# Performance work log

Hardware: AMD Instinct MI355X
Metric: run time of the kernel (lower is better)

## Reference

```python
import jax, jax.numpy as jnp
import numpy as np

K = 16          # neighbors per node
EPS = 1e-5      # BatchNorm eps
BN_SCALE = 1.0 / np.sqrt(1.0 + EPS)  # eval BN with running mean=0, var=1


def _knn_idx(x, k):
    # x: [B, N, d] -> idx [B, N, k] of k nearest neighbors (self excluded)
    sq = jnp.sum(x * x, axis=-1)                               # [B, N]
    d2 = sq[:, :, None] + sq[:, None, :] - 2.0 * jnp.einsum('bnd,bmd->bnm', x, x)
    n = x.shape[1]
    d2 = jnp.where(jnp.eye(n, dtype=bool)[None], jnp.inf, d2)  # no self loops
    _, idx = jax.lax.top_k(-d2, k)
    return idx


def _edge_conv(x, idx, W, b, g, be):
    # PyG EdgeConv: max_j MLP([x_i, x_j - x_i]); MLP = Linear+BN(eval)+ReLU
    xj = jax.vmap(lambda xb, ib: xb[ib])(x, idx)               # [B, N, k, d]
    xi = x[:, :, None, :]
    m = jnp.concatenate([jnp.broadcast_to(xi, xj.shape), xj - xi], axis=-1)
    h = m @ W + b                                              # [B, N, k, out]
    h = g * (h * BN_SCALE) + be                                # eval BatchNorm
    h = jax.nn.relu(h)
    return jnp.max(h, axis=2)                                  # scatter-max over k


def setup_inputs() -> dict:
    key = jax.random.key(0)
    ks = jax.random.split(key, 16)
    B, N, D, C = 128, 256, 6, 12

    def w(k_, shape, fan_in):
        return (jax.random.normal(k_, shape, jnp.float32) / np.sqrt(fan_in)).astype(jnp.float32)

    inp = {
        'x':   jax.random.normal(ks[0], (B, N, D), jnp.float32),
        'W1':  w(ks[1], (2 * 6, 64), 12),   'b1': jnp.zeros((64,), jnp.float32),
        'g1':  jnp.ones((64,), jnp.float32), 'be1': jnp.zeros((64,), jnp.float32),
        'W2':  w(ks[2], (2 * 64, 128), 128), 'b2': jnp.zeros((128,), jnp.float32),
        'g2':  jnp.ones((128,), jnp.float32), 'be2': jnp.zeros((128,), jnp.float32),
        'W3':  w(ks[3], (2 * 128, 256), 256), 'b3': jnp.zeros((256,), jnp.float32),
        'g3':  jnp.ones((256,), jnp.float32), 'be3': jnp.zeros((256,), jnp.float32),
        'Wf1': w(ks[4], (256, 128), 256),    'bf1': jnp.zeros((128,), jnp.float32),
        'gf':  jnp.ones((128,), jnp.float32), 'bef': jnp.zeros((128,), jnp.float32),
        'Wf2': w(ks[5], (128, C), 128),      'bf2': jnp.zeros((C,), jnp.float32),
    }
    return inp


def reference(x, W1, b1, g1, be1, W2, b2, g2, be2, W3, b3, g3, be3,
              Wf1, bf1, gf, bef, Wf2, bf2):
    h = _edge_conv(x, _knn_idx(x, K), W1, b1, g1, be1)   # [B, N, 64]
    h = _edge_conv(h, _knn_idx(h, K), W2, b2, g2, be2)   # [B, N, 128]
    h = _edge_conv(h, _knn_idx(h, K), W3, b3, g3, be3)   # [B, N, 256]
    p = jnp.max(h, axis=1)                               # global_max_pool [B, 256]
    f = jax.nn.relu(gf * ((p @ Wf1 + bf1) * BN_SCALE) + bef)
    return f @ Wf2 + bf2                                 # [B, num_classes]
```

## Files before the change

kernel.cpp:

```cpp
#include <hip/hip_runtime.h>
#include <cstdint>
#include <cstddef>

#define KNN 16
#define NPTS 256
#define NBATCH 128

static constexpr float BN_SCALE_F = 0.9999950000374997f;

__device__ inline unsigned int f32_ord(float f) {
    unsigned int u = __float_as_uint(f);
    return (u & 0x80000000u) ? ~u : (u | 0x80000000u);
}

__device__ __forceinline__ int wmap(int n) { return n + 4 * (n >> 4); }

template<int D>
__global__ __launch_bounds__(256) void sq_kernel(const float* __restrict__ x,
                                                 float* __restrict__ sq) {
    const int t = blockIdx.x * 256 + threadIdx.x;
    const float* r = x + (size_t)t * D;
    float s = 0.f;
    #pragma unroll
    for (int d = 0; d < D; ++d) s = fmaf(r[d], r[d], s);
    sq[t] = s;
}

template<int D>
__global__ __launch_bounds__(256) void gram_kernel(const float* __restrict__ x,
                                                   const float* __restrict__ sq,
                                                   float* __restrict__ d2) {
    constexpr int KS = (D >= 16) ? 16 : D;
    const int t  = threadIdx.x;
    const int tx = t & 15, ty = t >> 4;
    const int b    = blockIdx.x >> 4;
    const int tile = blockIdx.x & 15;
    const int i0 = (tile & 3) * 64;
    const int j0 = (tile >> 2) * 64;
    const int base = b * NPTS;

    __shared__ float As[KS][68];
    __shared__ float Bs[KS][68];

    float acc[4][4] = {};
    for (int k0 = 0; k0 < D; k0 += KS) {
        if constexpr (D % 16 == 0) {
            const int r  = t >> 2;
            const int cq = (t & 3) * 4;
            const float4 va = *(const float4*)(x + (size_t)(base + i0 + r) * D + k0 + cq);
            const float4 vb = *(const float4*)(x + (size_t)(base + j0 + r) * D + k0 + cq);
            As[cq + 0][r] = va.x; As[cq + 1][r] = va.y;
            As[cq + 2][r] = va.z; As[cq + 3][r] = va.w;
            Bs[cq + 0][r] = vb.x; Bs[cq + 1][r] = vb.y;
            Bs[cq + 2][r] = vb.z; Bs[cq + 3][r] = vb.w;
        } else {
            for (int e = t; e < 64 * KS; e += 256) {
                const int r = e / KS, c = e % KS;
                As[c][r] = x[(size_t)(base + i0 + r) * D + k0 + c];
                Bs[c][r] = x[(size_t)(base + j0 + r) * D + k0 + c];
            }
        }
        __syncthreads();
        #pragma unroll
        for (int kk = 0; kk < KS; ++kk) {
            const float4 av = *(const float4*)&As[kk][ty * 4];
            const float4 bv = *(const float4*)&Bs[kk][tx * 4];
            const float am[4] = {av.x, av.y, av.z, av.w};
            const float bm[4] = {bv.x, bv.y, bv.z, bv.w};
            #pragma unroll
            for (int m = 0; m < 4; ++m)
                #pragma unroll
                for (int n = 0; n < 4; ++n)
                    acc[m][n] = fmaf(am[m], bm[n], acc[m][n]);
        }
        __syncthreads();
    }

    float sqi[4], sqj[4];
    #pragma unroll
    for (int m = 0; m < 4; ++m) {
        sqi[m] = sq[base + i0 + ty * 4 + m];
        sqj[m] = sq[base + j0 + tx * 4 + m];
    }
    #pragma unroll
    for (int m = 0; m < 4; ++m) {
        const int gi = i0 + ty * 4 + m;
        float v[4];
        #pragma unroll
        for (int n = 0; n < 4; ++n) {
            v[n] = (sqi[m] + sqj[n]) - 2.f * acc[m][n];
            if (gi == j0 + tx * 4 + n) v[n] = INFINITY;
        }
        float4* dst = (float4*)(d2 + ((size_t)b << 16) + (size_t)gi * NPTS + j0 + tx * 4);
        *dst = make_float4(v[0], v[1], v[2], v[3]);
    }
}

__global__ __launch_bounds__(256) void topk_kernel(const float* __restrict__ d2,
                                                   int* __restrict__ idx) {
    const int t = threadIdx.x;
    const int p = t >> 3;
    const int q = t & 7;
    const int ig = blockIdx.x * 32 + p;
    const float* row = d2 + (size_t)ig * NPTS;

    unsigned long long L[16];
    #pragma unroll
    for (int r = 0; r < 16; ++r) L[r] = ~0ull;

    const int jb = q * 32;
    #pragma unroll
    for (int jj = 0; jj < 32; jj += 4) {
        const float4 v4 = *(const float4*)(row + jb + jj);
        const float vv[4] = {v4.x, v4.y, v4.z, v4.w};
        #pragma unroll
        for (int e = 0; e < 4; ++e) {
            const unsigned long long key =
                ((unsigned long long)f32_ord(vv[e]) << 32) |
                (unsigned int)(jb + jj + e);
            #pragma unroll
            for (int r = 15; r >= 1; --r)
                L[r] = (key < L[r]) ? ((key < L[r - 1]) ? L[r - 1] : key) : L[r];
            L[0] = (key < L[0]) ? key : L[0];
        }
    }

    __shared__ unsigned long long K[256][17];
    #pragma unroll
    for (int r = 0; r < 16; ++r) K[t][r] = L[r];
    __syncthreads();

    if (t < 32) {
        const int pp  = t;
        const int igo = blockIdx.x * 32 + pp;
        int h[8];
        unsigned long long v[8];
        #pragma unroll
        for (int c = 0; c < 8; ++c) { h[c] = 0; v[c] = K[pp * 8 + c][0]; }
        int outj[16];
        #pragma unroll
        for (int r = 0; r < 16; ++r) {
            unsigned long long best = v[0];
            #pragma unroll
            for (int c = 1; c < 8; ++c) best = (v[c] < best) ? v[c] : best;
            outj[r] = (int)(unsigned int)(best & 0xffffffffull);
            #pragma unroll
            for (int c = 0; c < 8; ++c) {
                const bool hit = (v[c] == best);
                const int hn = h[c] + (hit ? 1 : 0);
                const unsigned long long nv = K[pp * 8 + c][hn & 15];
                v[c] = hit ? ((hn < 16) ? nv : ~0ull) : v[c];
                h[c] = hn;
            }
        }
        int4* op = (int4*)(idx + (size_t)igo * KNN);
        op[0] = make_int4(outj[0],  outj[1],  outj[2],  outj[3]);
        op[1] = make_int4(outj[4],  outj[5],  outj[6],  outj[7]);
        op[2] = make_int4(outj[8],  outj[9],  outj[10], outj[11]);
        op[3] = make_int4(outj[12], outj[13], outj[14], outj[15]);
    }
}

template<int D, int C>
__global__ __launch_bounds__(256) void mlp_gemm_kernel(
        const float* __restrict__ x, const float* __restrict__ W,
        const float* __restrict__ bias, const float* __restrict__ g,
        const float* __restrict__ be,
        float* __restrict__ A, float* __restrict__ Bv) {
    constexpr int BM = 128;
    constexpr int KT = (D >= 16) ? 16 : D;
    const int t  = threadIdx.x;
    const int m0 = blockIdx.x * BM;
    const int n0 = blockIdx.y * 128;
    const int tx = t & 15;
    const int ty = t >> 4;

    __shared__ float Xs[KT][BM + 4];
    __shared__ float Ws[KT][160];

    float acc[8][8] = {};

    for (int k0 = 0; k0 < D; k0 += KT) {
        if constexpr (D % 16 == 0) {
            const int r  = t >> 1;
            const int cq = (t & 1) * 8;
            const float* src = x + (size_t)(m0 + r) * D + k0 + cq;
            const float4 v0 = *(const float4*)(src);
            const float4 v1 = *(const float4*)(src + 4);
            Xs[cq + 0][r] = v0.x; Xs[cq + 1][r] = v0.y;
            Xs[cq + 2][r] = v0.z; Xs[cq + 3][r] = v0.w;
            Xs[cq + 4][r] = v1.x; Xs[cq + 5][r] = v1.y;
            Xs[cq + 6][r] = v1.z; Xs[cq + 7][r] = v1.w;
        } else {
            for (int e = t; e < BM * KT; e += 256) {
                const int r = e / KT, c = e % KT;
                Xs[c][r] = x[(size_t)(m0 + r) * D + k0 + c];
            }
        }
        if constexpr (D % 16 == 0) {
            const int wk = t >> 4;
            const int nq = (t & 15) * 8;
            const int mb = wmap(nq);
            const int gn = n0 + nq;
            const int kr = k0 + wk;
            if (gn < C) {
                const float* pt = W + (size_t)kr * C + gn;
                const float* pb = W + (size_t)(D + kr) * C + gn;
                const float4 t0 = *(const float4*)(pt);
                const float4 t1 = *(const float4*)(pt + 4);
                const float4 b0 = *(const float4*)(pb);
                const float4 b1 = *(const float4*)(pb + 4);
                *(float4*)&Ws[wk][mb]     = make_float4(t0.x - b0.x, t0.y - b0.y,
                                                        t0.z - b0.z, t0.w - b0.w);
                *(float4*)&Ws[wk][mb + 4] = make_float4(t1.x - b1.x, t1.y - b1.y,
                                                        t1.z - b1.z, t1.w - b1.w);
            } else {
                const float* pb = W + (size_t)(D + kr) * C + (gn - C);
                *(float4*)&Ws[wk][mb]     = *(const float4*)(pb);
                *(float4*)&Ws[wk][mb + 4] = *(const float4*)(pb + 4);
            }
        } else {
            for (int e = t; e < KT * 128; e += 256) {
                const int k = e >> 7, n = e & 127;
                const int gn = n0 + n, kr = k0 + k;
                Ws[k][wmap(n)] = (gn < C)
                    ? W[(size_t)kr * C + gn] - W[(size_t)(D + kr) * C + gn]
                    : W[(size_t)(D + kr) * C + (gn - C)];
            }
        }
        __syncthreads();

        const int mc = wmap(tx * 8);
        #pragma unroll
        for (int kk = 0; kk < KT; ++kk) {
            float xm[8], wn[8];
            *(float4*)&xm[0] = *(const float4*)&Xs[kk][ty * 8];
            *(float4*)&xm[4] = *(const float4*)&Xs[kk][ty * 8 + 4];
            *(float4*)&wn[0] = *(const float4*)&Ws[kk][mc];
            *(float4*)&wn[4] = *(const float4*)&Ws[kk][mc + 4];
            #pragma unroll
            for (int m = 0; m < 8; ++m)
                #pragma unroll
                for (int n = 0; n < 8; ++n)
                    acc[m][n] = fmaf(xm[m], wn[n], acc[m][n]);
        }
        __syncthreads();
    }

    const int gn = n0 + tx * 8;
    if (gn < C) {
        float fac[8];
        #pragma unroll
        for (int e = 0; e < 8; ++e) fac[e] = g[gn + e] * BN_SCALE_F;
        #pragma unroll
        for (int m = 0; m < 8; ++m) {
            float o[8];
            #pragma unroll
            for (int e = 0; e < 8; ++e) o[e] = fac[e] * acc[m][e];
            float* dst = A + (size_t)(m0 + ty * 8 + m) * C + gn;
            *(float4*)(dst)     = make_float4(o[0], o[1], o[2], o[3]);
            *(float4*)(dst + 4) = make_float4(o[4], o[5], o[6], o[7]);
        }
    } else {
        const int cb = gn - C;
        float fac[8], bb[8], bee[8];
        #pragma unroll
        for (int e = 0; e < 8; ++e) {
            fac[e] = g[cb + e] * BN_SCALE_F;
            bb[e]  = bias[cb + e];
            bee[e] = be[cb + e];
        }
        #pragma unroll
        for (int m = 0; m < 8; ++m) {
            float o[8];
            #pragma unroll
            for (int e = 0; e < 8; ++e)
                o[e] = fmaf(fac[e], acc[m][e] + bb[e], bee[e]);
            float* dst = Bv + (size_t)(m0 + ty * 8 + m) * C + cb;
            *(float4*)(dst)     = make_float4(o[0], o[1], o[2], o[3]);
            *(float4*)(dst + 4) = make_float4(o[4], o[5], o[6], o[7]);
        }
    }
}

template<int C>
__global__ __launch_bounds__(C) void combine_kernel(
        const float* A, const float* __restrict__ Bv,
        const int* __restrict__ idx, float* out) {
    const int bi = blockIdx.x;
    const int c  = threadIdx.x;
    __shared__ int nbr[KNN];
    if (c < KNN) nbr[c] = idx[(size_t)bi * KNN + c];
    __syncthreads();
    const int b0 = bi & ~255;
    float mx = -INFINITY;
    #pragma unroll
    for (int kk = 0; kk < KNN; ++kk)
        mx = fmaxf(mx, Bv[(size_t)(b0 + nbr[kk]) * C + c]);
    float a = A[(size_t)bi * C + c];
    out[(size_t)bi * C + c] = fmaxf(a + mx, 0.f);
}

__global__ __launch_bounds__(256) void head_kernel(
        const float* __restrict__ h3, const float* __restrict__ Wf1,
        const float* __restrict__ bf1, const float* __restrict__ gf,
        const float* __restrict__ bef, const float* __restrict__ Wf2,
        const float* __restrict__ bf2, float* __restrict__ out) {
    const int b   = blockIdx.x;
    const int tid = threadIdx.x;
    __shared__ float p[256];
    __shared__ float f[128];
    const float* hb = h3 + (size_t)b * NPTS * 256;
    float mx = -INFINITY;
    for (int n = 0; n < NPTS; ++n) mx = fmaxf(mx, hb[(size_t)n * 256 + tid]);
    p[tid] = mx;
    __syncthreads();
    if (tid < 128) {
        float acc = bf1[tid];
        for (int d = 0; d < 256; ++d)
            acc = fmaf(p[d], Wf1[(size_t)d * 128 + tid], acc);
        float v = gf[tid] * (acc * BN_SCALE_F) + bef[tid];
        f[tid] = fmaxf(v, 0.f);
    }
    __syncthreads();
    if (tid < 12) {
        float acc = bf2[tid];
        for (int d = 0; d < 128; ++d)
            acc = fmaf(f[d], Wf2[(size_t)d * 12 + tid], acc);
        out[(size_t)b * 12 + tid] = acc;
    }
}

extern "C" void kernel_launch(void* const* d_in, const int* in_sizes, int n_in,
                              void* d_out, int out_size, void* d_ws, size_t ws_size,
                              hipStream_t stream) {
    const float* x   = (const float*)d_in[0];
    const float* W1  = (const float*)d_in[1];
    const float* b1  = (const float*)d_in[2];
    const float* g1  = (const float*)d_in[3];
    const float* be1 = (const float*)d_in[4];
    const float* W2  = (const float*)d_in[5];
    const float* b2  = (const float*)d_in[6];
    const float* g2  = (const float*)d_in[7];
    const float* be2 = (const float*)d_in[8];
    const float* W3  = (const float*)d_in[9];
    const float* b3  = (const float*)d_in[10];
    const float* g3  = (const float*)d_in[11];
    const float* be3 = (const float*)d_in[12];
    const float* Wf1 = (const float*)d_in[13];
    const float* bf1 = (const float*)d_in[14];
    const float* gf  = (const float*)d_in[15];
    const float* bef = (const float*)d_in[16];
    const float* Wf2 = (const float*)d_in[17];
    const float* bf2 = (const float*)d_in[18];
    float* out = (float*)d_out;

    char* ws = (char*)d_ws;
    const size_t idx_bytes = (size_t)NBATCH * NPTS * KNN * sizeof(int);
    const size_t reg_bytes = (size_t)NBATCH * NPTS * 256 * sizeof(float);
    int*   idx = (int*)ws;
    float* R1  = (float*)(ws + idx_bytes);
    float* R2  = (float*)(ws + idx_bytes + reg_bytes);
    float* R3  = (float*)(ws + idx_bytes + 2 * reg_bytes);
    float* sqb = (float*)(ws + idx_bytes + 3 * reg_bytes);

    const int BN = NBATCH * NPTS;
    const int GRAM_GRID = NBATCH * 16;
    const int TOPK_GRID = BN / 32;
    const int MB = BN / 128;

    sq_kernel<6><<<BN / 256, 256, 0, stream>>>(x, sqb);
    gram_kernel<6><<<GRAM_GRID, 256, 0, stream>>>(x, sqb, R3);
    topk_kernel<<<TOPK_GRID, 256, 0, stream>>>(R3, idx);
    mlp_gemm_kernel<6, 64><<<dim3(MB, 1), 256, 0, stream>>>(
        x, W1, b1, g1, be1, R1, R2);
    combine_kernel<64><<<BN, 64, 0, stream>>>(R1, R2, idx, R1);

    sq_kernel<64><<<BN / 256, 256, 0, stream>>>(R1, sqb);
    gram_kernel<64><<<GRAM_GRID, 256, 0, stream>>>(R1, sqb, R3);
    topk_kernel<<<TOPK_GRID, 256, 0, stream>>>(R3, idx);
    mlp_gemm_kernel<64, 128><<<dim3(MB, 2), 256, 0, stream>>>(
        R1, W2, b2, g2, be2, R2, R3);
    combine_kernel<128><<<BN, 128, 0, stream>>>(R2, R3, idx, R2);

    sq_kernel<128><<<BN / 256, 256, 0, stream>>>(R2, sqb);
    gram_kernel<128><<<GRAM_GRID, 256, 0, stream>>>(R2, sqb, R1);
    topk_kernel<<<TOPK_GRID, 256, 0, stream>>>(R1, idx);
    mlp_gemm_kernel<128, 256><<<dim3(MB, 4), 256, 0, stream>>>(
        R2, W3, b3, g3, be3, R3, R1);
    combine_kernel<256><<<BN, 256, 0, stream>>>(R3, R1, idx, R3);

    head_kernel<<<NBATCH, 256, 0, stream>>>(R3, Wf1, bf1, gf, bef, Wf2, bf2, out);
}
```

Baseline: 482.1 us.

## Fuse distance matrix and top-k selection into one kNN kernel

Replaces the separate gram kernel (which wrote the full 256x256 distance matrix per batch to global memory) and the top-k kernel (which read it back) with a single kernel. Each block owns 64 query rows, loops over four 64-column tiles, stages distances in shared memory, and keeps per-thread sorted top-16 lists using 32-bit keys plus separate indices, then merges four partial lists per row. This removes the d2 global round trip and a launch per layer. In exchange the grid shrinks from 2048 to 512 blocks, shared memory use grows, and register pressure rises, which may reduce occupancy.

Measured after the change: 463.3 us. -3.9%, faster.

```diff
diff --git a/kernel.cpp b/kernel.cpp
--- a/kernel.cpp
+++ b/kernel.cpp
@@ -27,133 +27,143 @@
 }
 
 template<int D>
-__global__ __launch_bounds__(256) void gram_kernel(const float* __restrict__ x,
-                                                   const float* __restrict__ sq,
-                                                   float* __restrict__ d2) {
+__global__ __launch_bounds__(256) void knn_fused_kernel(
+        const float* __restrict__ x, const float* __restrict__ sq,
+        int* __restrict__ idx) {
     constexpr int KS = (D >= 16) ? 16 : D;
     const int t  = threadIdx.x;
     const int tx = t & 15, ty = t >> 4;
-    const int b    = blockIdx.x >> 4;
-    const int tile = blockIdx.x & 15;
-    const int i0 = (tile & 3) * 64;
-    const int j0 = (tile >> 2) * 64;
+    const int sr = t >> 2, sc = t & 3;
+    const int b  = blockIdx.x >> 2;
+    const int i0 = (blockIdx.x & 3) * 64;
     const int base = b * NPTS;
 
     __shared__ float As[KS][68];
     __shared__ float Bs[KS][68];
-
-    float acc[4][4] = {};
-    for (int k0 = 0; k0 < D; k0 += KS) {
-        if constexpr (D % 16 == 0) {
-            const int r  = t >> 2;
-            const int cq = (t & 3) * 4;
-            const float4 va = *(const float4*)(x + (size_t)(base + i0 + r) * D + k0 + cq);
-            const float4 vb = *(const float4*)(x + (size_t)(base + j0 + r) * D + k0 + cq);
-            As[cq + 0][r] = va.x; As[cq + 1][r] = va.y;
-            As[cq + 2][r] = va.z; As[cq + 3][r] = va.w;
-            Bs[cq + 0][r] = vb.x; Bs[cq + 1][r] = vb.y;
-            Bs[cq + 2][r] = vb.z; Bs[cq + 3][r] = vb.w;
-        } else {
-            for (int e = t; e < 64 * KS; e += 256) {
-                const int r = e / KS, c = e % KS;
-                As[c][r] = x[(size_t)(base + i0 + r) * D + k0 + c];
-                Bs[c][r] = x[(size_t)(base + j0 + r) * D + k0 + c];
+    __shared__ float d2L[64][65];
+    __shared__ unsigned short Mi[64][68];
+
+    unsigned int Lv[16], Li[16];
+    #pragma unroll
+    for (int q = 0; q < 16; ++q) { Lv[q] = 0xFFFFFFFFu; Li[q] = 0u; }
+
+    for (int jt = 0; jt < 4; ++jt) {
+        const int j0 = jt * 64;
+        float acc[4][4] = {};
+        for (int k0 = 0; k0 < D; k0 += KS) {
+            if constexpr (D % 16 == 0) {
+                const int r  = t >> 2;
+                const int cq = (t & 3) * 4;
+                const float4 va = *(const float4*)(x + (size_t)(base + i0 + r) * D + k0 + cq);
+                const float4 vb = *(const float4*)(x + (size_t)(base + j0 + r) * D + k0 + cq);
+                As[cq + 0][r] = va.x; As[cq + 1][r] = va.y;
+                As[cq + 2][r] = va.z; As[cq + 3][r] = va.w;
+                Bs[cq + 0][r] = vb.x; Bs[cq + 1][r] = vb.y;
+                Bs[cq + 2][r] = vb.z; Bs[cq + 3][r] = vb.w;
+            } else {
+                for (int e = t; e < 64 * KS; e += 256) {
+                    const int r = e / KS, c = e % KS;
+                    As[c][r] = x[(size_t)(base + i0 + r) * D + k0 + c];
+                    Bs[c][r] = x[(size_t)(base + j0 + r) * D + k0 + c];
+                }
+            }
+            __syncthreads();
+            #pragma unroll
+            for (int kk = 0; kk < KS; ++kk) {
+                const float4 av = *(const float4*)&As[kk][ty * 4];
+                const float4 bv = *(const float4*)&Bs[kk][tx * 4];
+                const float am[4] = {av.x, av.y, av.z, av.w};
+                const float bm[4] = {bv.x, bv.y, bv.z, bv.w};
+                #pragma unroll
+                for (int m = 0; m < 4; ++m)
+                    #pragma unroll
+                    for (int n = 0; n < 4; ++n)
+                        acc[m][n] = fmaf(am[m], bm[n], acc[m][n]);
+            }
+            __syncthreads();
+        }
+
+        float sqi[4], sqj[4];
+        #pragma unroll
+        for (int m = 0; m < 4; ++m) {
+            sqi[m] = sq[base + i0 + ty * 4 + m];
+            sqj[m] = sq[base + j0 + tx * 4 + m];
+        }
+        #pragma unroll
+        for (int m = 0; m < 4; ++m) {
+            const int gi = i0 + ty * 4 + m;
+            #pragma unroll
+            for (int n = 0; n < 4; ++n) {
+                float v = (sqi[m] + sqj[n]) - 2.f * acc[m][n];
+                if (gi == j0 + tx * 4 + n) v = INFINITY;
+                d2L[ty * 4 + m][tx * 4 + n] = v;
             }
         }
         __syncthreads();
-        #pragma unroll
-        for (int kk = 0; kk < KS; ++kk) {
-            const float4 av = *(const float4*)&As[kk][ty * 4];
-            const float4 bv = *(const float4*)&Bs[kk][tx * 4];
-            const float am[4] = {av.x, av.y, av.z, av.w};
-            const float bm[4] = {bv.x, bv.y, bv.z, bv.w};
-            #pragma unroll
-            for (int m = 0; m < 4; ++m)
-                #pragma unroll
-                for (int n = 0; n < 4; ++n)
-                    acc[m][n] = fmaf(am[m], bm[n], acc[m][n]);
-        }
-        __syncthreads();
-    }
-
-    float sqi[4], sqj[4];
+
+        #pragma unroll
+        for (int i = 0; i < 16; ++i) {
+            const unsigned int v = f32_ord(d2L[sr][sc * 16 + i]);
+            const unsigned int j = (unsigned int)(j0 + sc * 16 + i);
+            #pragma unroll
+            for (int q = 15; q >= 1; --q) {
+                const bool a = v < Lv[q];
+                const bool c = v < Lv[q - 1];
+                Lv[q] = a ? (c ? Lv[q - 1] : v) : Lv[q];
+                Li[q] = a ? (c ? Li[q - 1] : j) : Li[q];
+            }
+            const bool a0 = v < Lv[0];
+            Lv[0] = a0 ? v : Lv[0];
+            Li[0] = a0 ? j : Li[0];
+        }
+    }
+
+    __syncthreads();
     #pragma unroll
-    for (int m = 0; m < 4; ++m) {
-        sqi[m] = sq[base + i0 + ty * 4 + m];
-        sqj[m] = sq[base + j0 + tx * 4 + m];
-    }
-    #pragma unroll
-    for (int m = 0; m < 4; ++m) {
-        const int gi = i0 + ty * 4 + m;
-        float v[4];
-        #pragma unroll
-        for (int n = 0; n < 4; ++n) {
-            v[n] = (sqi[m] + sqj[n]) - 2.f * acc[m][n];
-            if (gi == j0 + tx * 4 + n) v[n] = INFINITY;
-        }
-        float4* dst = (float4*)(d2 + ((size_t)b << 16) + (size_t)gi * NPTS + j0 + tx * 4);
-        *dst = make_float4(v[0], v[1], v[2], v[3]);
-    }
-}
-
-__global__ __launch_bounds__(256) void topk_kernel(const float* __restrict__ d2,
-                                                   int* __restrict__ idx) {
-    const int t = threadIdx.x;
-    const int p = t >> 3;
-    const int q = t & 7;
-    const int ig = blockIdx.x * 32 + p;
-    const float* row = d2 + (size_t)ig * NPTS;
-
-    unsigned long long L[16];
-    #pragma unroll
-    for (int r = 0; r < 16; ++r) L[r] = ~0ull;
-
-    const int jb = q * 32;
-    #pragma unroll
-    for (int jj = 0; jj < 32; jj += 4) {
-        const float4 v4 = *(const float4*)(row + jb + jj);
-        const float vv[4] = {v4.x, v4.y, v4.z, v4.w};
-        #pragma unroll
-        for (int e = 0; e < 4; ++e) {
-            const unsigned long long key =
-                ((unsigned long long)f32_ord(vv[e]) << 32) |
-                (unsigned int)(jb + jj + e);
-            #pragma unroll
-            for (int r = 15; r >= 1; --r)
-                L[r] = (key < L[r]) ? ((key < L[r - 1]) ? L[r - 1] : key) : L[r];
-            L[0] = (key < L[0]) ? key : L[0];
-        }
-    }
-
-    __shared__ unsigned long long K[256][17];
-    #pragma unroll
-    for (int r = 0; r < 16; ++r) K[t][r] = L[r];
+    for (int q = 0; q < 16; ++q) {
+        d2L[sr][sc * 16 + q] = __uint_as_float(Lv[q]);
+        Mi[sr][sc * 16 + q]  = (unsigned short)Li[q];
+    }
     __syncthreads();
 
-    if (t < 32) {
-        const int pp  = t;
-        const int igo = blockIdx.x * 32 + pp;
-        int h[8];
-        unsigned long long v[8];
-        #pragma unroll
-        for (int c = 0; c < 8; ++c) { h[c] = 0; v[c] = K[pp * 8 + c][0]; }
+    if (t < 64) {
+        const int row = t;
+        int h[4];
+        unsigned int cv[4], ci[4];
+        #pragma unroll
+        for (int c = 0; c < 4; ++c) {
+            h[c]  = 0;
+            cv[c] = __float_as_uint(d2L[row][c * 16]);
+            ci[c] = Mi[row][c * 16];
+        }
         int outj[16];
         #pragma unroll
-        for (int r = 0; r < 16; ++r) {
-            unsigned long long best = v[0];
-            #pragma unroll
-            for (int c = 1; c < 8; ++c) best = (v[c] < best) ? v[c] : best;
-            outj[r] = (int)(unsigned int)(best & 0xffffffffull);
-            #pragma unroll
-            for (int c = 0; c < 8; ++c) {
-                const bool hit = (v[c] == best);
-                const int hn = h[c] + (hit ? 1 : 0);
-                const unsigned long long nv = K[pp * 8 + c][hn & 15];
-                v[c] = hit ? ((hn < 16) ? nv : ~0ull) : v[c];
-                h[c] = hn;
-            }
-        }
-        int4* op = (int4*)(idx + (size_t)igo * KNN);
+        for (int rd = 0; rd < 16; ++rd) {
+            unsigned int bv = cv[0], bi = ci[0];
+            int bc = 0;
+            #pragma unroll
+            for (int c = 1; c < 4; ++c) {
+                const bool tk = (cv[c] < bv) | ((cv[c] == bv) & (ci[c] < bi));
+                bv = tk ? cv[c] : bv;
+                bi = tk ? ci[c] : bi;
+                bc = tk ? c     : bc;
+            }
+            outj[rd] = (int)bi;
+            #pragma unroll
+            for (int c = 0; c < 4; ++c) {
+                if (c == bc) {
+                    const int hn = h[c] + 1;
+                    h[c] = hn;
+                    if (hn < 16) {
+                        cv[c] = __float_as_uint(d2L[row][c * 16 + hn]);
+                        ci[c] = Mi[row][c * 16 + hn];
+                    } else {
+                        cv[c] = 0xFFFFFFFFu;
+                    }
+                }
+            }
+        }
+        int4* op = (int4*)(idx + (size_t)(base + i0 + row) * KNN);
         op[0] = make_int4(outj[0],  outj[1],  outj[2],  outj[3]);
         op[1] = make_int4(outj[4],  outj[5],  outj[6],  outj[7]);
         op[2] = make_int4(outj[8],  outj[9],  outj[10], outj[11]);
@@ -365,27 +375,23 @@
     float* sqb = (float*)(ws + idx_bytes + 3 * reg_bytes);
 
     const int BN = NBATCH * NPTS;
-    const int GRAM_GRID = NBATCH * 16;
-    const int TOPK_GRID = BN / 32;
+    const int KNN_GRID = NBATCH * 4;
     const int MB = BN / 128;
 
     sq_kernel<6><<<BN / 256, 256, 0, stream>>>(x, sqb);
-    gram_kernel<6><<<GRAM_GRID, 256, 0, stream>>>(x, sqb, R3);
-    topk_kernel<<<TOPK_GRID, 256, 0, stream>>>(R3, idx);
+    knn_fused_kernel<6><<<KNN_GRID, 256, 0, stream>>>(x, sqb, idx);
     mlp_gemm_kernel<6, 64><<<dim3(MB, 1), 256, 0, stream>>>(
         x, W1, b1, g1, be1, R1, R2);
     combine_kernel<64><<<BN, 64, 0, stream>>>(R1, R2, idx, R1);
 
     sq_kernel<64><<<BN / 256, 256, 0, stream>>>(R1, sqb);
-    gram_kernel<64><<<GRAM_GRID, 256, 0, stream>>>(R1, sqb, R3);
-    topk_kernel<<<TOPK_GRID, 256, 0, stream>>>(R3, idx);
+    knn_fused_kernel<64><<<KNN_GRID, 256, 0, stream>>>(R1, sqb, idx);
     mlp_gemm_kernel<64, 128><<<dim3(MB, 2), 256, 0, stream>>>(
         R1, W2, b2, g2, be2, R2, R3);
     combine_kernel<128><<<BN, 128, 0, stream>>>(R2, R3, idx, R2);
 
     sq_kernel<128><<<BN / 256, 256, 0, stream>>>(R2, sqb);
-    gram_kernel<128><<<GRAM_GRID, 256, 0, stream>>>(R2, sqb, R1);
-    topk_kernel<<<TOPK_GRID, 256, 0, stream>>>(R1, idx);
+    knn_fused_kernel<128><<<KNN_GRID, 256, 0, stream>>>(R2, sqb, idx);
     mlp_gemm_kernel<128, 256><<<dim3(MB, 4), 256, 0, stream>>>(
         R2, W3, b3, g3, be3, R3, R1);
     combine_kernel<256><<<BN, 256, 0, stream>>>(R3, R1, idx, R3);
```
